# Optimization experiments

Hardware: AMD Instinct MI355X
Metric: run time of the kernel (lower is better)

Reference implementation:

```python
import jax, jax.numpy as jnp
import numpy as np

B, S, D, H = 4, 2048, 1024, 16
HD = D // H

def setup_inputs() -> dict:
    key = jax.random.key(0)
    ks = jax.random.split(key, 11)
    s = 1.0 / np.sqrt(D)
    def lin(k):
        kw, kb = jax.random.split(k)
        return (jax.random.uniform(kw, (D, D), jnp.float32, -s, s),
                jax.random.uniform(kb, (D,), jnp.float32, -s, s))
    Wq, bq = lin(ks[0]); Wk, bk = lin(ks[1]); Wv, bv = lin(ks[2]); Wo, bo = lin(ks[3])
    return {
        "query": jax.random.normal(ks[4], (B, S, D), jnp.float32),
        "key": jax.random.normal(ks[5], (B, S, D), jnp.float32),
        "value": jax.random.normal(ks[6], (B, S, D), jnp.float32),
        "Wq": Wq, "bq": bq, "Wk": Wk, "bk": bk,
        "Wv": Wv, "bv": bv, "Wo": Wo, "bo": bo,
    }

def reference(query, key, value, Wq, bq, Wk, bk, Wv, bv, Wo, bo):
    def split_heads(x):  # [B,S,D] -> [B,H,S,HD]
        return x.reshape(B, S, H, HD).transpose(0, 2, 1, 3)
    q = split_heads(query @ Wq + bq)
    k = split_heads(key @ Wk + bk)
    v = split_heads(value @ Wv + bv)
    scores = jnp.einsum('bhqd,bhkd->bhqk', q, k) / np.sqrt(HD)
    probs = jax.nn.softmax(scores, axis=-1)
    ctx = jnp.einsum('bhqk,bhkd->bhqd', probs, v)
    ctx = ctx.transpose(0, 2, 1, 3).reshape(B, S, D)
    return ctx @ Wo + bo
```

## Files before the change

### kernel.cpp

```cpp
#include <hip/hip_runtime.h>
#include <hip/hip_bf16.h>

#define B_ 4
#define S_ 2048
#define D_ 1024
#define H_ 16
#define HD_ 64
#define M_ (B_*S_)

typedef __bf16 bf16;
typedef bf16 bf16x8 __attribute__((ext_vector_type(8)));
typedef bf16 bf16x4 __attribute__((ext_vector_type(4)));
typedef bf16 bf16x2 __attribute__((ext_vector_type(2)));
typedef float f32x4 __attribute__((ext_vector_type(4)));
typedef unsigned u32x4 __attribute__((ext_vector_type(4)));

__device__ __forceinline__ void gload_lds16(const void* g, void* l) {
  __builtin_amdgcn_global_load_lds((const __attribute__((address_space(1))) void*)g,
                                   (__attribute__((address_space(3))) void*)l, 16, 0, 0);
}

__device__ __forceinline__ unsigned pk2(float a, float b) {
  bf16x2 v;
  v[0] = (bf16)a; v[1] = (bf16)b;
  return __builtin_bit_cast(unsigned, v);
}

__global__ __launch_bounds__(256)
void wtrans_kernel(const float* __restrict__ Wq, const float* __restrict__ Wk,
                   const float* __restrict__ Wv, const float* __restrict__ Wo,
                   bf16* __restrict__ Wqt, bf16* __restrict__ Wkt,
                   bf16* __restrict__ Wvt, bf16* __restrict__ Wot) {
  __shared__ float tile[64][65];
  const float* W; bf16* Wt;
  switch (blockIdx.z) {
    case 0: W = Wq; Wt = Wqt; break;
    case 1: W = Wk; Wt = Wkt; break;
    case 2: W = Wv; Wt = Wvt; break;
    default: W = Wo; Wt = Wot; break;
  }
  int n0 = blockIdx.x * 64, k0 = blockIdx.y * 64;
  int tx = threadIdx.x & 63, ty = threadIdx.x >> 6;
#pragma unroll
  for (int i = 0; i < 16; i++) {
    int k = ty + i * 4;
    tile[k][tx] = W[(size_t)(k0 + k) * D_ + n0 + tx];
  }
  __syncthreads();
#pragma unroll
  for (int i = 0; i < 16; i++) {
    int n = ty + i * 4;
    Wt[(size_t)(n0 + n) * D_ + k0 + tx] = (bf16)tile[tx][n];
  }
}

__global__ __launch_bounds__(256)
void qkv_cvt_kernel(const float* __restrict__ q, const float* __restrict__ k,
                    const float* __restrict__ v,
                    bf16* __restrict__ qo, bf16* __restrict__ ko, bf16* __restrict__ vo) {
  const float* src; bf16* dst;
  switch (blockIdx.y) {
    case 0: src = q; dst = qo; break;
    case 1: src = k; dst = ko; break;
    default: src = v; dst = vo; break;
  }
  size_t i = ((size_t)blockIdx.x * 256 + threadIdx.x) * 8;
  f32x4 a = *(const f32x4*)(src + i);
  f32x4 b = *(const f32x4*)(src + i + 4);
  bf16x8 o;
  o[0] = (bf16)a[0]; o[1] = (bf16)a[1]; o[2] = (bf16)a[2]; o[3] = (bf16)a[3];
  o[4] = (bf16)b[0]; o[5] = (bf16)b[1]; o[6] = (bf16)b[2]; o[7] = (bf16)b[3];
  *(bf16x8*)(dst + i) = o;
}

#define QSCALE 0.18033688011112042f

__global__ __launch_bounds__(256)
void proj_gemm_kernel(const bf16* __restrict__ Aqb, const bf16* __restrict__ Akb,
                      const bf16* __restrict__ Avb,
                      const bf16* __restrict__ Wqt, const bf16* __restrict__ Wkt,
                      const bf16* __restrict__ Wvt,
                      const float* __restrict__ bq, const float* __restrict__ bk,
                      const float* __restrict__ bv,
                      bf16* __restrict__ qb, bf16* __restrict__ kb, bf16* __restrict__ vbT) {
  __shared__ bf16 As[128 * 64];
  __shared__ bf16 Bs[128 * 64];
  const bf16* A; const bf16* Bt; const float* bias;
  if (blockIdx.z == 0)      { A = Aqb; Bt = Wqt; bias = bq; }
  else if (blockIdx.z == 1) { A = Akb; Bt = Wkt; bias = bk; }
  else                      { A = Avb; Bt = Wvt; bias = bv; }

  const int orig = blockIdx.y * gridDim.x + blockIdx.x;
  const int swz  = (orig & 7) * 64 + (orig >> 3);
  const int n0 = (swz & 7) * 128, m0 = (swz >> 3) * 128;

  const int tid = threadIdx.x;
  const int lane = tid & 63, w = tid >> 6;
  const int wr = w >> 1, wc = w & 1;
  const int l15 = lane & 15, quad = lane >> 4;
  const int srow = lane >> 3, schunk = lane & 7;

  f32x4 acc[4][4] = {};

  for (int kt = 0; kt < D_ / 64; kt++) {
    const int k0 = kt * 64;
#pragma unroll
    for (int t = 0; t < 4; t++) {
      int r0 = w * 32 + t * 8;
      int row = r0 + srow;
      int cg = schunk ^ (row & 7);
      gload_lds16(A + (size_t)(m0 + row) * D_ + k0 + cg * 8, &As[r0 * 64]);
      gload_lds16(Bt + (size_t)(n0 + row) * D_ + k0 + cg * 8, &Bs[r0 * 64]);
    }
    __syncthreads();

#pragma unroll
    for (int ks = 0; ks < 2; ks++) {
      bf16x8 a[4], b[4];
#pragma unroll
      for (int fm = 0; fm < 4; fm++) {
        int row = wr * 64 + fm * 16 + l15;
        a[fm] = *(const bf16x8*)(&As[row * 64 + (((ks * 4 + quad) ^ (row & 7)) * 8)]);
      }
#pragma unroll
      for (int fn = 0; fn < 4; fn++) {
        int row = wc * 64 + fn * 16 + l15;
        b[fn] = *(const bf16x8*)(&Bs[row * 64 + (((ks * 4 + quad) ^ (row & 7)) * 8)]);
      }
#pragma unroll
      for (int fm = 0; fm < 4; fm++)
#pragma unroll
        for (int fn = 0; fn < 4; fn++)
          acc[fm][fn] = __builtin_amdgcn_mfma_f32_16x16x32_bf16(a[fm], b[fn], acc[fm][fn], 0, 0, 0);
    }
    __syncthreads();
  }

  if (blockIdx.z < 2) {
    bf16* C = (blockIdx.z == 0) ? qb : kb;
    float scale = (blockIdx.z == 0) ? QSCALE : 1.0f;
#pragma unroll
    for (int fm = 0; fm < 4; fm++) {
      int row = m0 + wr * 64 + fm * 16 + quad * 4;
#pragma unroll
      for (int fn = 0; fn < 4; fn++) {
        int col = n0 + wc * 64 + fn * 16 + l15;
        float bval = bias[col];
#pragma unroll
        for (int r = 0; r < 4; r++)
          C[(size_t)(row + r) * D_ + col] = (bf16)((acc[fm][fn][r] + bval) * scale);
      }
    }
  } else {
#pragma unroll
    for (int fm = 0; fm < 4; fm++) {
      int row = m0 + wr * 64 + fm * 16 + quad * 4;
#pragma unroll
      for (int fn = 0; fn < 4; fn++) {
        int col = n0 + wc * 64 + fn * 16 + l15;
        float bval = bias[col];
        bf16x4 pk;
#pragma unroll
        for (int r = 0; r < 4; r++) pk[r] = (bf16)(acc[fm][fn][r] + bval);
        *(bf16x4*)(vbT + (size_t)col * M_ + row) = pk;
      }
    }
  }
}

__global__ __launch_bounds__(256)
void attn_kernel(const bf16* __restrict__ qb, const bf16* __restrict__ kb,
                 const bf16* __restrict__ vbT, bf16* __restrict__ ctxb) {
  __shared__ bf16 Ks[2][64 * 64];
  __shared__ bf16 Vs[2][64 * 64];

  const int orig = blockIdx.y * gridDim.x + blockIdx.x;
  const int swz  = (orig & 7) * 128 + (orig >> 3);
  const int bh = swz >> 4;
  const int b = bh >> 4, h = bh & 15;
  const int q0 = (swz & 15) * 128;

  const int tid = threadIdx.x, lane = tid & 63, w = tid >> 6;
  const int l15 = lane & 15, quad = lane >> 4;

  const size_t baseQ = ((size_t)(b * S_ + q0)) * D_ + h * HD_;

  bf16x8 qf[2][2];
#pragma unroll
  for (int fm = 0; fm < 2; fm++)
#pragma unroll
    for (int ks = 0; ks < 2; ks++)
      qf[fm][ks] = *(const bf16x8*)(qb + baseQ + (size_t)(w * 32 + fm * 16 + l15) * D_ + ks * 32 + quad * 8);

  bf16x8 vones;
#pragma unroll
  for (int i = 0; i < 8; i++) vones[i] = (bf16)1.0f;

  f32x4 o[2][4] = {};
  f32x4 o_l[2] = {};

  const int srow_i = lane >> 3;
  const int schunk = lane & 7;

  auto stage = [&](int buf, int kt) {
#pragma unroll
    for (int t = 0; t < 2; t++) {
      const int r0 = w * 16 + t * 8;
      const int row = r0 + srow_i;
      const int c = schunk ^ (row & 7);
      const bf16* gK = kb + ((size_t)(b * S_ + kt * 64 + row)) * D_ + h * 64 + c * 8;
      gload_lds16(gK, &Ks[buf][r0 * 64]);
      const bf16* gV = vbT + ((size_t)(h * 64 + row)) * M_ + b * S_ + kt * 64 + c * 8;
      gload_lds16(gV, &Vs[buf][r0 * 64]);
    }
  };

  stage(0, 0);
  __syncthreads();

  for (int kt = 0; kt < S_ / 64; kt++) {
    const int buf = kt & 1;
    if (kt + 1 < S_ / 64) stage(buf ^ 1, kt + 1);

    f32x4 st[4][2] = {};
    __builtin_amdgcn_s_setprio(1);
#pragma unroll
    for (int ks = 0; ks < 2; ks++) {
#pragma unroll
      for (int fk = 0; fk < 4; fk++) {
        const int key = fk * 16 + l15;
        bf16x8 kf = *(const bf16x8*)(&Ks[buf][key * 64 + (((ks * 4 + quad) ^ (key & 7)) * 8)]);
#pragma unroll
        for (int fq = 0; fq < 2; fq++)
          st[fk][fq] = __builtin_amdgcn_mfma_f32_16x16x32_bf16(kf, qf[fq][ks], st[fk][fq], 0, 0, 0);
      }
    }
    __builtin_amdgcn_s_setprio(0);

#pragma unroll
    for (int fk = 0; fk < 4; fk++)
#pragma unroll
      for (int fq = 0; fq < 2; fq++) {
        st[fk][fq][0] = __builtin_amdgcn_exp2f(st[fk][fq][0]);
        st[fk][fq][1] = __builtin_amdgcn_exp2f(st[fk][fq][1]);
        st[fk][fq][2] = __builtin_amdgcn_exp2f(st[fk][fq][2]);
        st[fk][fq][3] = __builtin_amdgcn_exp2f(st[fk][fq][3]);
      }

#pragma unroll
    for (int ks2 = 0; ks2 < 2; ks2++) {
      bf16x8 pf[2], vf[4];
#pragma unroll
      for (int fm = 0; fm < 2; fm++) {
        unsigned A0 = pk2(st[2 * ks2][fm][0], st[2 * ks2][fm][1]);
        unsigned A1 = pk2(st[2 * ks2][fm][2], st[2 * ks2][fm][3]);
        unsigned B0 = pk2(st[2 * ks2 + 1][fm][0], st[2 * ks2 + 1][fm][1]);
        unsigned B1 = pk2(st[2 * ks2 + 1][fm][2], st[2 * ks2 + 1][fm][3]);
        auto s0 = __builtin_amdgcn_permlane32_swap(A0, B0, false, false);
        auto s1 = __builtin_amdgcn_permlane32_swap(A1, B1, false, false);
        auto t0 = __builtin_amdgcn_permlane16_swap(s0[0], s0[1], false, false);
        auto t1 = __builtin_amdgcn_permlane16_swap(s1[0], s1[1], false, false);
        u32x4 wv;
        wv[0] = t0[0]; wv[1] = t1[0]; wv[2] = t0[1]; wv[3] = t1[1];
        pf[fm] = __builtin_bit_cast(bf16x8, wv);
      }
#pragma unroll
      for (int fd = 0; fd < 4; fd++) {
        const int d = fd * 16 + l15;
        vf[fd] = *(const bf16x8*)(&Vs[buf][d * 64 + (((ks2 * 4 + quad) ^ (d & 7)) * 8)]);
      }
      __builtin_amdgcn_s_setprio(1);
#pragma unroll
      for (int fm = 0; fm < 2; fm++) {
#pragma unroll
        for (int fd = 0; fd < 4; fd++)
          o[fm][fd] = __builtin_amdgcn_mfma_f32_16x16x32_bf16(pf[fm], vf[fd], o[fm][fd], 0, 0, 0);
        o_l[fm] = __builtin_amdgcn_mfma_f32_16x16x32_bf16(pf[fm], vones, o_l[fm], 0, 0, 0);
      }
      __builtin_amdgcn_s_setprio(0);
    }
    __syncthreads();
  }

#pragma unroll
  for (int fm = 0; fm < 2; fm++) {
#pragma unroll
    for (int r = 0; r < 4; r++) {
      float inv = 1.0f / o_l[fm][r];
      int row = w * 32 + fm * 16 + quad * 4 + r;
#pragma unroll
      for (int fd = 0; fd < 4; fd++)
        ctxb[baseQ + (size_t)row * D_ + fd * 16 + l15] = (bf16)(o[fm][fd][r] * inv);
    }
  }
}

__global__ __launch_bounds__(256)
void out_gemm_kernel(const bf16* __restrict__ A, const bf16* __restrict__ Bt,
                     const float* __restrict__ bias, float* __restrict__ Cout) {
  __shared__ bf16 As[128 * 64];
  __shared__ bf16 Bs[128 * 64];
  const int orig = blockIdx.y * gridDim.x + blockIdx.x;
  const int swz  = (orig & 7) * 64 + (orig >> 3);
  const int n0 = (swz & 7) * 128, m0 = (swz >> 3) * 128;

  const int tid = threadIdx.x;
  const int lane = tid & 63, w = tid >> 6;
  const int wr = w >> 1, wc = w & 1;
  const int l15 = lane & 15, quad = lane >> 4;
  const int srow = lane >> 3, schunk = lane & 7;

  f32x4 acc[4][4] = {};

  for (int kt = 0; kt < D_ / 64; kt++) {
    const int k0 = kt * 64;
#pragma unroll
    for (int t = 0; t < 4; t++) {
      int r0 = w * 32 + t * 8;
      int row = r0 + srow;
      int cg = schunk ^ (row & 7);
      gload_lds16(A + (size_t)(m0 + row) * D_ + k0 + cg * 8, &As[r0 * 64]);
      gload_lds16(Bt + (size_t)(n0 + row) * D_ + k0 + cg * 8, &Bs[r0 * 64]);
    }
    __syncthreads();

#pragma unroll
    for (int ks = 0; ks < 2; ks++) {
      bf16x8 a[4], b[4];
#pragma unroll
      for (int fm = 0; fm < 4; fm++) {
        int row = wr * 64 + fm * 16 + l15;
        a[fm] = *(const bf16x8*)(&As[row * 64 + (((ks * 4 + quad) ^ (row & 7)) * 8)]);
      }
#pragma unroll
      for (int fn = 0; fn < 4; fn++) {
        int row = wc * 64 + fn * 16 + l15;
        b[fn] = *(const bf16x8*)(&Bs[row * 64 + (((ks * 4 + quad) ^ (row & 7)) * 8)]);
      }
#pragma unroll
      for (int fm = 0; fm < 4; fm++)
#pragma unroll
        for (int fn = 0; fn < 4; fn++)
          acc[fm][fn] = __builtin_amdgcn_mfma_f32_16x16x32_bf16(a[fm], b[fn], acc[fm][fn], 0, 0, 0);
    }
    __syncthreads();
  }
#pragma unroll
  for (int fm = 0; fm < 4; fm++) {
    int row = m0 + wr * 64 + fm * 16 + quad * 4;
#pragma unroll
    for (int fn = 0; fn < 4; fn++) {
      int col = n0 + wc * 64 + fn * 16 + l15;
      float bval = bias[col];
#pragma unroll
      for (int r = 0; r < 4; r++)
        Cout[(size_t)(row + r) * D_ + col] = acc[fm][fn][r] + bval;
    }
  }
}

extern "C" void kernel_launch(void* const* d_in, const int* in_sizes, int n_in,
                              void* d_out, int out_size, void* d_ws, size_t ws_size,
                              hipStream_t stream) {
  const float* query = (const float*)d_in[0];
  const float* key   = (const float*)d_in[1];
  const float* value = (const float*)d_in[2];
  const float* Wq = (const float*)d_in[3];
  const float* bq = (const float*)d_in[4];
  const float* Wk = (const float*)d_in[5];
  const float* bk = (const float*)d_in[6];
  const float* Wv = (const float*)d_in[7];
  const float* bv = (const float*)d_in[8];
  const float* Wo = (const float*)d_in[9];
  const float* bo = (const float*)d_in[10];
  float* out = (float*)d_out;

  char* ws = (char*)d_ws;
  const size_t WT_BYTES = (size_t)D_ * D_ * sizeof(bf16);
  const size_t MD_BYTES = (size_t)M_ * D_ * sizeof(bf16);
  bf16* Wqt  = (bf16*)(ws);
  bf16* Wkt  = (bf16*)(ws + WT_BYTES);
  bf16* Wvt  = (bf16*)(ws + 2 * WT_BYTES);
  bf16* Wot  = (bf16*)(ws + 3 * WT_BYTES);
  bf16* qb   = (bf16*)(ws + 4 * WT_BYTES);
  bf16* kb   = (bf16*)(ws + 4 * WT_BYTES + MD_BYTES);
  bf16* vbT  = (bf16*)(ws + 4 * WT_BYTES + 2 * MD_BYTES);
  bf16* ctxb = (bf16*)(ws + 4 * WT_BYTES + 3 * MD_BYTES);
  bf16* qcv  = ctxb;
  bf16* kcv  = (bf16*)(ws + 4 * WT_BYTES + 4 * MD_BYTES);
  bf16* vcv  = (bf16*)(ws + 4 * WT_BYTES + 5 * MD_BYTES);

  wtrans_kernel<<<dim3(D_ / 64, D_ / 64, 4), 256, 0, stream>>>(
      Wq, Wk, Wv, Wo, Wqt, Wkt, Wvt, Wot);

  qkv_cvt_kernel<<<dim3((size_t)M_ * D_ / 2048, 3), 256, 0, stream>>>(
      query, key, value, qcv, kcv, vcv);

  proj_gemm_kernel<<<dim3(D_ / 128, M_ / 128, 3), 256, 0, stream>>>(
      qcv, kcv, vcv, Wqt, Wkt, Wvt, bq, bk, bv, qb, kb, vbT);

  attn_kernel<<<dim3(S_ / 128, B_ * H_), 256, 0, stream>>>(qb, kb, vbT, ctxb);

  out_gemm_kernel<<<dim3(D_ / 128, M_ / 128), 256, 0, stream>>>(ctxb, Wot, bo, out);
}
```

Measured before the change: 351.6 us.

## Software-pipeline attention: overlap next tile's QK with previous tile's softmax·V

The attention loop is restructured so the QK^T MFMAs for tile t run in the same iteration as the exp, pack and PV MFMAs of tile t-1, using two score register sets. The V shared-memory buffer is tripled because V must survive one extra iteration. The goal is to interleave matrix-core work with the exp/permute VALU work and hide LDS latency. In exchange, register pressure rises with the two score sets, which could lower occupancy or cause spills, and LDS use grows.

```diff
diff --git a/kernel.cpp b/kernel.cpp
--- a/kernel.cpp
+++ b/kernel.cpp
@@ -168,11 +168,13 @@
   }
 }
 
+#define NT_ (S_ / 64)
+
 __global__ __launch_bounds__(256)
 void attn_kernel(const bf16* __restrict__ qb, const bf16* __restrict__ kb,
                  const bf16* __restrict__ vbT, bf16* __restrict__ ctxb) {
   __shared__ bf16 Ks[2][64 * 64];
-  __shared__ bf16 Vs[2][64 * 64];
+  __shared__ bf16 Vs[3][64 * 64];
 
   const int orig = blockIdx.y * gridDim.x + blockIdx.x;
   const int swz  = (orig & 7) * 128 + (orig >> 3);
@@ -202,41 +204,42 @@
   const int srow_i = lane >> 3;
   const int schunk = lane & 7;
 
-  auto stage = [&](int buf, int kt) {
+  auto stage = [&](int kt) {
+    if (kt >= NT_) return;
+    const int kbuf = kt & 1, vbuf = kt % 3;
 #pragma unroll
     for (int t = 0; t < 2; t++) {
       const int r0 = w * 16 + t * 8;
       const int row = r0 + srow_i;
       const int c = schunk ^ (row & 7);
       const bf16* gK = kb + ((size_t)(b * S_ + kt * 64 + row)) * D_ + h * 64 + c * 8;
-      gload_lds16(gK, &Ks[buf][r0 * 64]);
+      gload_lds16(gK, &Ks[kbuf][r0 * 64]);
       const bf16* gV = vbT + ((size_t)(h * 64 + row)) * M_ + b * S_ + kt * 64 + c * 8;
-      gload_lds16(gV, &Vs[buf][r0 * 64]);
+      gload_lds16(gV, &Vs[vbuf][r0 * 64]);
     }
   };
 
-  stage(0, 0);
-  __syncthreads();
-
-  for (int kt = 0; kt < S_ / 64; kt++) {
-    const int buf = kt & 1;
-    if (kt + 1 < S_ / 64) stage(buf ^ 1, kt + 1);
-
-    f32x4 st[4][2] = {};
+  auto QK = [&](f32x4 (&st)[4][2], int kbuf) {
+#pragma unroll
+    for (int fk = 0; fk < 4; fk++)
+#pragma unroll
+      for (int fq = 0; fq < 2; fq++) st[fk][fq] = f32x4{};
     __builtin_amdgcn_s_setprio(1);
 #pragma unroll
     for (int ks = 0; ks < 2; ks++) {
 #pragma unroll
       for (int fk = 0; fk < 4; fk++) {
         const int key = fk * 16 + l15;
-        bf16x8 kf = *(const bf16x8*)(&Ks[buf][key * 64 + (((ks * 4 + quad) ^ (key & 7)) * 8)]);
+        bf16x8 kf = *(const bf16x8*)(&Ks[kbuf][key * 64 + (((ks * 4 + quad) ^ (key & 7)) * 8)]);
 #pragma unroll
         for (int fq = 0; fq < 2; fq++)
           st[fk][fq] = __builtin_amdgcn_mfma_f32_16x16x32_bf16(kf, qf[fq][ks], st[fk][fq], 0, 0, 0);
       }
     }
     __builtin_amdgcn_s_setprio(0);
-
+  };
+
+  auto FIN = [&](f32x4 (&st)[4][2], int vbuf) {
 #pragma unroll
     for (int fk = 0; fk < 4; fk++)
 #pragma unroll
@@ -246,7 +249,6 @@
         st[fk][fq][2] = __builtin_amdgcn_exp2f(st[fk][fq][2]);
         st[fk][fq][3] = __builtin_amdgcn_exp2f(st[fk][fq][3]);
       }
-
 #pragma unroll
     for (int ks2 = 0; ks2 < 2; ks2++) {
       bf16x8 pf[2], vf[4];
@@ -267,7 +269,7 @@
 #pragma unroll
       for (int fd = 0; fd < 4; fd++) {
         const int d = fd * 16 + l15;
-        vf[fd] = *(const bf16x8*)(&Vs[buf][d * 64 + (((ks2 * 4 + quad) ^ (d & 7)) * 8)]);
+        vf[fd] = *(const bf16x8*)(&Vs[vbuf][d * 64 + (((ks2 * 4 + quad) ^ (d & 7)) * 8)]);
       }
       __builtin_amdgcn_s_setprio(1);
 #pragma unroll
@@ -279,8 +281,25 @@
       }
       __builtin_amdgcn_s_setprio(0);
     }
-    __syncthreads();
-  }
+  };
+
+  f32x4 stA[4][2], stB[4][2];
+
+  stage(0);
+  __syncthreads();
+
+  for (int i = 0; i < NT_ / 2; i++) {
+    const int t = 2 * i;
+    stage(t + 1);
+    QK(stA, t & 1);
+    if (i > 0) FIN(stB, (t - 1) % 3);
+    __syncthreads();
+    stage(t + 2);
+    QK(stB, (t + 1) & 1);
+    FIN(stA, t % 3);
+    __syncthreads();
+  }
+  FIN(stB, (NT_ - 1) % 3);
 
 #pragma unroll
   for (int fm = 0; fm < 2; fm++) {
```

Result: faster. 334.4 us (median of 3 runs) (-4.9%).
